# Kernel tuning notes

Measured on AMD Instinct MI355X. Metric: run time of the kernel, lower is better.

Reference implementation:

```python
import jax, jax.numpy as jnp
import numpy as np

HIDDEN = 1024
NUM_HEADS = 16
HEAD_DIM = HIDDEN // NUM_HEADS


def setup_inputs() -> dict:
    key = jax.random.key(0)
    ks = jax.random.split(key, 13)
    B, S, H = 4, 2048, HIDDEN
    sc = 1.0 / np.sqrt(H)
    inp = {
        'queries': jax.random.normal(ks[0], (B, S, H), jnp.float32),
        'keys': jax.random.normal(ks[1], (B, S, H), jnp.float32),
        'values': jax.random.normal(ks[2], (B, S, H), jnp.float32),
        'attention_mask': jax.random.randint(ks[3], (B, S, S), 0, 2, jnp.int32),
        'W_q': jax.random.normal(ks[4], (H, H), jnp.float32) * sc,
        'b_q': jnp.zeros((H,), jnp.float32),
        'W_k': jax.random.normal(ks[5], (H, H), jnp.float32) * sc,
        'b_k': jnp.zeros((H,), jnp.float32),
        'W_v': jax.random.normal(ks[6], (H, H), jnp.float32) * sc,
        'b_v': jnp.zeros((H,), jnp.float32),
        'W_o': jax.random.normal(ks[7], (H, H), jnp.float32) * sc,
        'b_o': jnp.zeros((H,), jnp.float32),
    }
    return inp


def _split_heads(x):
    # [B, S, H] -> [B, nH, S, d]
    B, S, _ = x.shape
    return x.reshape(B, S, NUM_HEADS, HEAD_DIM).transpose(0, 2, 1, 3)


def reference(queries, keys, values, attention_mask, W_q, b_q, W_k, b_k, W_v, b_v, W_o, b_o):
    q = _split_heads(queries @ W_q + b_q)   # [B, nH, S, d]
    k = _split_heads(keys @ W_k + b_k)
    v = _split_heads(values @ W_v + b_v)
    d = q.shape[-1]
    scores = jnp.einsum('bhqd,bhkd->bhqk', q, k) / jnp.sqrt(jnp.float32(d))
    # mask repeat_interleave over heads == broadcast mask over head axis
    mask = attention_mask[:, None, :, :]    # [B, 1, S, S]
    scores = jnp.where(mask == 0, jnp.float32(-1e6), scores)
    attn = jax.nn.softmax(scores, axis=-1)  # dropout p=0 -> identity
    out = jnp.einsum('bhqk,bhkd->bhqd', attn, v)  # [B, nH, S, d]
    B, _, S, _ = out.shape
    out = out.transpose(0, 2, 1, 3).reshape(B, S, NUM_HEADS * HEAD_DIM)
    return out @ W_o + b_o
```

## Files before the change

kernel.cpp:

```cpp
#include <hip/hip_runtime.h>
#include <stdint.h>

typedef unsigned short u16;
typedef uint32_t u32;
typedef unsigned long long u64;
typedef short bf16x8 __attribute__((ext_vector_type(8)));
typedef float f32x4 __attribute__((ext_vector_type(4)));
typedef float f32x16 __attribute__((ext_vector_type(16)));

#define MFMA16 __builtin_amdgcn_mfma_f32_16x16x32_bf16
#define MFMA32 __builtin_amdgcn_mfma_f32_32x32x16_bf16
#define L2E 1.44269504088896340736f

static __device__ __forceinline__ u16 f2bf(float f) {
  union { float f; u32 u; } v; v.f = f;
  u32 r = v.u + 0x7FFFu + ((v.u >> 16) & 1u);
  return (u16)(r >> 16);
}

static __device__ __forceinline__ u32 cvtpk(float lo, float hi) {
  u32 r;
  asm("v_cvt_pk_bf16_f32 %0, %1, %2" : "=v"(r) : "v"(lo), "v"(hi));
  return r;
}

static __device__ __forceinline__ void glds16(const u16* g, u16* l) {
  __builtin_amdgcn_global_load_lds((const __attribute__((address_space(1))) void*)g,
                                   (__attribute__((address_space(3))) void*)l, 16, 0, 0);
}

__global__ __launch_bounds__(256) void cvt3_kernel(
    const float* __restrict__ s0, const float* __restrict__ s1, const float* __restrict__ s2,
    u16* __restrict__ d0, u16* __restrict__ d1, u16* __restrict__ d2) {
  const float* s = (blockIdx.z == 0) ? s0 : (blockIdx.z == 1) ? s1 : s2;
  u16* d = (blockIdx.z == 0) ? d0 : (blockIdx.z == 1) ? d1 : d2;
  size_t i = ((size_t)blockIdx.x * 256 + threadIdx.x) * 8;
  float4 a = *(const float4*)(s + i);
  float4 c = *(const float4*)(s + i + 4);
  bf16x8 o;
  o[0] = (short)f2bf(a.x); o[1] = (short)f2bf(a.y);
  o[2] = (short)f2bf(a.z); o[3] = (short)f2bf(a.w);
  o[4] = (short)f2bf(c.x); o[5] = (short)f2bf(c.y);
  o[6] = (short)f2bf(c.z); o[7] = (short)f2bf(c.w);
  *(bf16x8*)(d + i) = o;
}

__global__ __launch_bounds__(256) void wtrans_kernel(
    const float* __restrict__ w0, const float* __restrict__ w1,
    const float* __restrict__ w2, const float* __restrict__ w3,
    u16* __restrict__ t0, u16* __restrict__ t1, u16* __restrict__ t2, u16* __restrict__ t3) {
  const float* w = (blockIdx.z == 0) ? w0 : (blockIdx.z == 1) ? w1 : (blockIdx.z == 2) ? w2 : w3;
  u16* t = (blockIdx.z == 0) ? t0 : (blockIdx.z == 1) ? t1 : (blockIdx.z == 2) ? t2 : t3;
  __shared__ float tile[64][65];
  const int bx = blockIdx.x, by = blockIdx.y;
#pragma unroll
  for (int i = 0; i < 16; ++i) {
    int idx = i * 256 + threadIdx.x;
    int r = idx >> 6, c = idx & 63;
    tile[r][c] = w[(size_t)(by * 64 + r) * 1024 + bx * 64 + c];
  }
  __syncthreads();
#pragma unroll
  for (int i = 0; i < 16; ++i) {
    int idx = i * 256 + threadIdx.x;
    int r = idx >> 6, c = idx & 63;
    t[(size_t)(bx * 64 + r) * 1024 + by * 64 + c] = f2bf(tile[c][r]);
  }
}

__global__ __launch_bounds__(256) void packmask_kernel(const int* __restrict__ m,
                                                       u32* __restrict__ pmo) {
  const size_t i = (size_t)blockIdx.x * 256 + threadIdx.x;
  const int lane = threadIdx.x & 63;
  unsigned long long b = __ballot(m[i] != 0);
  if (lane == 0) pmo[i >> 5] = (u32)b;
  else if (lane == 32) pmo[i >> 5] = (u32)(b >> 32);
}

template <int OM>
__global__ __launch_bounds__(512, 2) void gemm_kernel(
    const u16* __restrict__ A, const u16* __restrict__ Bt, const float* __restrict__ bias,
    void* __restrict__ Cout, float oscale) {
  constexpr int K = 1024, N = 1024;
  constexpr int NT = K / 64;
  __shared__ u16 As[3][256 * 64];
  __shared__ u16 Bs[3][128 * 64];
  const int tid = threadIdx.x;
  const int lane = tid & 63;
  const int wid = tid >> 6;
  const int l15 = lane & 15;
  const int lg = lane >> 4;
  const int row0 = blockIdx.x * 256;
  const int col0 = blockIdx.y * 128;
  const int wr = wid >> 1, wc = wid & 1;
  const int swf = (l15 & 7) << 3;
  const f32x4 fzero = {0.f, 0.f, 0.f, 0.f};

  f32x4 acc[4][4];
#pragma unroll
  for (int m = 0; m < 4; ++m)
#pragma unroll
    for (int n = 0; n < 4; ++n) acc[m][n] = fzero;

#define GSTAGE(buf, k0)                                                        \
  do {                                                                         \
    _Pragma("unroll") for (int i = 0; i < 4; ++i) {                            \
      int e = (i * 512 + tid) * 8;                                             \
      int r = e >> 6, c = e & 63;                                              \
      int cs = c ^ ((r & 7) << 3);                                             \
      glds16(A + (size_t)(row0 + r) * K + (k0) + cs, &As[buf][e]);             \
    }                                                                          \
    _Pragma("unroll") for (int i = 0; i < 2; ++i) {                            \
      int e = (i * 512 + tid) * 8;                                             \
      int r = e >> 6, c = e & 63;                                              \
      int cs = c ^ ((r & 7) << 3);                                             \
      glds16(Bt + (size_t)(col0 + r) * K + (k0) + cs, &Bs[buf][e]);            \
    }                                                                          \
  } while (0)

  GSTAGE(0, 0);
  GSTAGE(1, 64);
  asm volatile("s_waitcnt vmcnt(6)" ::: "memory");
  __builtin_amdgcn_s_barrier();
  __builtin_amdgcn_sched_barrier(0);

  for (int t = 0; t < NT; ++t) {
    const int buf = t % 3;
    if (t + 2 < NT) GSTAGE((t + 2) % 3, (t + 2) * 64);

    __builtin_amdgcn_s_setprio(1);
#pragma unroll
    for (int ks = 0; ks < 2; ++ks) {
      const int koff = ks * 32 + lg * 8;
      bf16x8 af[4], bfr[4];
#pragma unroll
      for (int m = 0; m < 4; ++m)
        af[m] = *(const bf16x8*)(&As[buf][(wr * 64 + m * 16 + l15) * 64 + (koff ^ swf)]);
#pragma unroll
      for (int n = 0; n < 4; ++n)
        bfr[n] = *(const bf16x8*)(&Bs[buf][(wc * 64 + n * 16 + l15) * 64 + (koff ^ swf)]);
#pragma unroll
      for (int m = 0; m < 4; ++m)
#pragma unroll
        for (int n = 0; n < 4; ++n)
          acc[m][n] = MFMA16(af[m], bfr[n], acc[m][n], 0, 0, 0);
    }
    __builtin_amdgcn_s_setprio(0);

    if (t + 1 < NT) {
      if (t + 2 < NT)
        asm volatile("s_waitcnt vmcnt(6)" ::: "memory");
      else
        asm volatile("s_waitcnt vmcnt(0)" ::: "memory");
      __builtin_amdgcn_s_barrier();
      __builtin_amdgcn_sched_barrier(0);
    }
  }
#undef GSTAGE

#pragma unroll
  for (int n = 0; n < 4; ++n) {
    const int col = col0 + wc * 64 + n * 16 + l15;
    const float bv = bias[col];
#pragma unroll
    for (int m = 0; m < 4; ++m) {
#pragma unroll
      for (int r = 0; r < 4; ++r) {
        const int row = row0 + wr * 64 + m * 16 + lg * 4 + r;
        const float v = (acc[m][n][r] + bv) * oscale;
        if constexpr (OM == 0) {
          ((u16*)Cout)[(size_t)row * N + col] = f2bf(v);
        } else if constexpr (OM == 1) {
          ((float*)Cout)[(size_t)row * N + col] = v;
        } else {
          const int b_ = row >> 11, s_ = row & 2047, h_ = col >> 6, d_ = col & 63;
          ((u16*)Cout)[(size_t)((b_ * 16 + h_) * 64 + d_) * 2048 + s_] = f2bf(v);
        }
      }
    }
  }
}

__global__ __launch_bounds__(256, 4) void attn_kernel(
    const u16* __restrict__ Qb, const u16* __restrict__ Kb, const u16* __restrict__ Vt,
    const u32* __restrict__ pm, u16* __restrict__ Oa) {
  __shared__ u16 Ks[2][64 * 64];
  __shared__ u16 Vs[2][64 * 64];
  __shared__ uint4 mlut[16];
  const int tid = threadIdx.x;
  const int lane = tid & 63;
  const int wid = tid >> 6;
  const int c31 = lane & 31;
  const int hi = lane >> 5;
  const int qt = blockIdx.x;
  const int hh = blockIdx.y;
  const int bb = blockIdx.z;
  const int qbase = qt * 128 + wid * 32;
  const int sw = (lane & 7) << 3;

  if (tid < 16)
    mlut[tid] = make_uint4((u32) - (int)(tid & 1), (u32) - (int)((tid >> 1) & 1),
                           (u32) - (int)((tid >> 2) & 1), (u32) - (int)((tid >> 3) & 1));

  const size_t qrow = (size_t)(bb * 2048 + qbase + c31);
  bf16x8 qf[4];
#pragma unroll
  for (int ds = 0; ds < 4; ++ds)
    qf[ds] = *(const bf16x8*)(Qb + qrow * 1024 + hh * 64 + ds * 16 + hi * 8);

  float lrun = 0.f;
  f32x16 oacc[2];
#pragma unroll
  for (int dn = 0; dn < 2; ++dn)
#pragma unroll
    for (int r = 0; r < 16; ++r) oacc[dn][r] = 0.f;

  const size_t kgbase = (size_t)(bb * 2048) * 1024 + hh * 64;
  const size_t vgbase = (size_t)((bb * 16 + hh) * 64) * 2048;

#define STAGE(buf, kbase)                                                              \
  do {                                                                                 \
    _Pragma("unroll") for (int i = 0; i < 2; ++i) {                                    \
      int r = ((i * 256 + tid) * 8) >> 6, c = ((i * 256 + tid) * 8) & 63;              \
      int cs = c ^ ((r & 7) << 3);                                                     \
      glds16(Kb + kgbase + (size_t)((kbase) + r) * 1024 + cs,                          \
             &Ks[buf][(i * 256 + wid * 64) * 8]);                                      \
      glds16(Vt + vgbase + (size_t)r * 2048 + (kbase) + cs,                            \
             &Vs[buf][(i * 256 + wid * 64) * 8]);                                      \
    }                                                                                  \
  } while (0)

  STAGE(0, 0);
  __syncthreads();

  int cur = 0;
  for (int kt = 0; kt < 32; ++kt) {
    if (kt < 31) STAGE(cur ^ 1, (kt + 1) * 64);

    const u64 mw = *(const u64*)(pm + qrow * 64 + kt * 2);
    float ps = 0.f;

#pragma unroll
    for (int kb = 0; kb < 2; ++kb) {
      f32x16 sacc;
#pragma unroll
      for (int r = 0; r < 16; ++r) sacc[r] = 0.f;
#pragma unroll
      for (int ds = 0; ds < 4; ++ds) {
        bf16x8 kf = *(const bf16x8*)(&Ks[cur][(kb * 32 + c31) * 64 + ((ds * 16 + hi * 8) ^ sw)]);
        sacc = MFMA32(kf, qf[ds], sacc, 0, 0, 0);
      }

      const u32 mwk = (u32)(mw >> (kb * 32));
      u32 Ap[4], Bp[4];
#pragma unroll
      for (int q2 = 0; q2 < 4; ++q2) {
        const u32 kb4 = (mwk >> (q2 * 8 + hi * 4)) & 0xFu;
        const uint4 mm = mlut[kb4];
        const float p0 = __builtin_amdgcn_exp2f(sacc[4 * q2 + 0]);
        const float p1 = __builtin_amdgcn_exp2f(sacc[4 * q2 + 1]);
        const float p2 = __builtin_amdgcn_exp2f(sacc[4 * q2 + 2]);
        const float p3 = __builtin_amdgcn_exp2f(sacc[4 * q2 + 3]);
        const float f0 = __uint_as_float(__float_as_uint(p0) & mm.x);
        const float f1 = __uint_as_float(__float_as_uint(p1) & mm.y);
        const float f2 = __uint_as_float(__float_as_uint(p2) & mm.z);
        const float f3 = __uint_as_float(__float_as_uint(p3) & mm.w);
        ps += (f0 + f1) + (f2 + f3);
        Ap[q2] = cvtpk(f0, f1);
        Bp[q2] = cvtpk(f2, f3);
      }

      asm("v_permlane32_swap_b32 %0, %1" : "+v"(Ap[0]), "+v"(Ap[1]));
      asm("v_permlane32_swap_b32 %0, %1" : "+v"(Bp[0]), "+v"(Bp[1]));
      asm("v_permlane32_swap_b32 %0, %1" : "+v"(Ap[2]), "+v"(Ap[3]));
      asm("v_permlane32_swap_b32 %0, %1" : "+v"(Bp[2]), "+v"(Bp[3]));

#pragma unroll
      for (int t = 0; t < 2; ++t) {
        uint4 fr;
        fr.x = Ap[2 * t]; fr.y = Bp[2 * t]; fr.z = Ap[2 * t + 1]; fr.w = Bp[2 * t + 1];
        const bf16x8 pf = *(const bf16x8*)&fr;
        const int koff = (kb * 2 + t) * 16 + hi * 8;
#pragma unroll
        for (int dn = 0; dn < 2; ++dn) {
          bf16x8 vf = *(const bf16x8*)(&Vs[cur][(dn * 32 + c31) * 64 + (koff ^ sw)]);
          oacc[dn] = MFMA32(vf, pf, oacc[dn], 0, 0, 0);
        }
      }
    }

    ps += __shfl_xor(ps, 32);
    lrun += ps;

    __syncthreads();
    cur ^= 1;
  }
#undef STAGE

  const float inv = 1.0f / lrun;
  u16* orow = Oa + qrow * 1024 + hh * 64;
#pragma unroll
  for (int dn = 0; dn < 2; ++dn) {
#pragma unroll
    for (int q2 = 0; q2 < 4; ++q2) {
      uint2 w;
      w.x = cvtpk(oacc[dn][4 * q2 + 0] * inv, oacc[dn][4 * q2 + 1] * inv);
      w.y = cvtpk(oacc[dn][4 * q2 + 2] * inv, oacc[dn][4 * q2 + 3] * inv);
      *(uint2*)(orow + dn * 32 + q2 * 8 + hi * 4) = w;
    }
  }
}

extern "C" void kernel_launch(void* const* d_in, const int* in_sizes, int n_in,
                              void* d_out, int out_size, void* d_ws, size_t ws_size,
                              hipStream_t stream) {
  const float* q = (const float*)d_in[0];
  const float* k = (const float*)d_in[1];
  const float* v = (const float*)d_in[2];
  const int* mask = (const int*)d_in[3];
  const float* Wq = (const float*)d_in[4]; const float* bq = (const float*)d_in[5];
  const float* Wk = (const float*)d_in[6]; const float* bk = (const float*)d_in[7];
  const float* Wv = (const float*)d_in[8]; const float* bv = (const float*)d_in[9];
  const float* Wo = (const float*)d_in[10]; const float* bo = (const float*)d_in[11];
  float* out = (float*)d_out;
  char* ws = (char*)d_ws;
  const size_t MB = 1024ull * 1024ull;
  u16* qbf = (u16*)(ws + 0 * MB);
  u16* kbf = (u16*)(ws + 16 * MB);
  u16* vbf = (u16*)(ws + 32 * MB);
  u16* Qp  = (u16*)(ws + 48 * MB);
  u16* Kp  = (u16*)(ws + 64 * MB);
  u16* Vtp = (u16*)(ws + 80 * MB);
  u16* Wqt = (u16*)(ws + 96 * MB);
  u16* Wkt = (u16*)(ws + 98 * MB);
  u16* Wvt = (u16*)(ws + 100 * MB);
  u16* Wot = (u16*)(ws + 102 * MB);
  u32* pmb = (u32*)(ws + 104 * MB);
  u16* Oa  = qbf;

  const float QSCALE = 0.125f * L2E;

  cvt3_kernel<<<dim3(4096, 1, 3), 256, 0, stream>>>(q, k, v, qbf, kbf, vbf);
  wtrans_kernel<<<dim3(16, 16, 4), 256, 0, stream>>>(Wq, Wk, Wv, Wo, Wqt, Wkt, Wvt, Wot);
  packmask_kernel<<<dim3(65536), 256, 0, stream>>>(mask, pmb);
  gemm_kernel<0><<<dim3(32, 8), 512, 0, stream>>>(qbf, Wqt, bq, Qp, QSCALE);
  gemm_kernel<0><<<dim3(32, 8), 512, 0, stream>>>(kbf, Wkt, bk, Kp, 1.0f);
  gemm_kernel<2><<<dim3(32, 8), 512, 0, stream>>>(vbf, Wvt, bv, Vtp, 1.0f);
  attn_kernel<<<dim3(16, 16, 4), 256, 0, stream>>>(Qp, Kp, Vtp, pmb, Oa);
  gemm_kernel<1><<<dim3(32, 8), 512, 0, stream>>>(Oa, Wot, bo, out, 1.0f);
}
```

Baseline: 267.6 us.

## Fuse fp32-to-bf16 input conversion into projection GEMM A-tile loads

```diff
diff --git a/kernel.cpp b/kernel.cpp
--- a/kernel.cpp
+++ b/kernel.cpp
@@ -27,22 +27,6 @@
 static __device__ __forceinline__ void glds16(const u16* g, u16* l) {
   __builtin_amdgcn_global_load_lds((const __attribute__((address_space(1))) void*)g,
                                    (__attribute__((address_space(3))) void*)l, 16, 0, 0);
-}
-
-__global__ __launch_bounds__(256) void cvt3_kernel(
-    const float* __restrict__ s0, const float* __restrict__ s1, const float* __restrict__ s2,
-    u16* __restrict__ d0, u16* __restrict__ d1, u16* __restrict__ d2) {
-  const float* s = (blockIdx.z == 0) ? s0 : (blockIdx.z == 1) ? s1 : s2;
-  u16* d = (blockIdx.z == 0) ? d0 : (blockIdx.z == 1) ? d1 : d2;
-  size_t i = ((size_t)blockIdx.x * 256 + threadIdx.x) * 8;
-  float4 a = *(const float4*)(s + i);
-  float4 c = *(const float4*)(s + i + 4);
-  bf16x8 o;
-  o[0] = (short)f2bf(a.x); o[1] = (short)f2bf(a.y);
-  o[2] = (short)f2bf(a.z); o[3] = (short)f2bf(a.w);
-  o[4] = (short)f2bf(c.x); o[5] = (short)f2bf(c.y);
-  o[6] = (short)f2bf(c.z); o[7] = (short)f2bf(c.w);
-  *(bf16x8*)(d + i) = o;
 }
 
 __global__ __launch_bounds__(256) void wtrans_kernel(
@@ -79,12 +63,15 @@
 
 template <int OM>
 __global__ __launch_bounds__(512, 2) void gemm_kernel(
-    const u16* __restrict__ A, const u16* __restrict__ Bt, const float* __restrict__ bias,
+    const void* __restrict__ Apv, const u16* __restrict__ Bt, const float* __restrict__ bias,
     void* __restrict__ Cout, float oscale) {
   constexpr int K = 1024, N = 1024;
   constexpr int NT = K / 64;
+  constexpr bool AF32 = (OM != 1);
   __shared__ u16 As[3][256 * 64];
   __shared__ u16 Bs[3][128 * 64];
+  const u16* Ab = (const u16*)Apv;
+  const float* Af = (const float*)Apv;
   const int tid = threadIdx.x;
   const int lane = tid & 63;
   const int wid = tid >> 6;
@@ -102,14 +89,10 @@
 #pragma unroll
     for (int n = 0; n < 4; ++n) acc[m][n] = fzero;
 
-#define GSTAGE(buf, k0)                                                        \
+  float4 aA[8], aB[8];
+
+#define BGLDS(buf, k0)                                                         \
   do {                                                                         \
-    _Pragma("unroll") for (int i = 0; i < 4; ++i) {                            \
-      int e = (i * 512 + tid) * 8;                                             \
-      int r = e >> 6, c = e & 63;                                              \
-      int cs = c ^ ((r & 7) << 3);                                             \
-      glds16(A + (size_t)(row0 + r) * K + (k0) + cs, &As[buf][e]);             \
-    }                                                                          \
     _Pragma("unroll") for (int i = 0; i < 2; ++i) {                            \
       int e = (i * 512 + tid) * 8;                                             \
       int r = e >> 6, c = e & 63;                                              \
@@ -118,45 +101,130 @@
     }                                                                          \
   } while (0)
 
-  GSTAGE(0, 0);
-  GSTAGE(1, 64);
-  asm volatile("s_waitcnt vmcnt(6)" ::: "memory");
-  __builtin_amdgcn_s_barrier();
-  __builtin_amdgcn_sched_barrier(0);
-
-  for (int t = 0; t < NT; ++t) {
-    const int buf = t % 3;
-    if (t + 2 < NT) GSTAGE((t + 2) % 3, (t + 2) * 64);
-
-    __builtin_amdgcn_s_setprio(1);
-#pragma unroll
-    for (int ks = 0; ks < 2; ++ks) {
-      const int koff = ks * 32 + lg * 8;
-      bf16x8 af[4], bfr[4];
-#pragma unroll
-      for (int m = 0; m < 4; ++m)
-        af[m] = *(const bf16x8*)(&As[buf][(wr * 64 + m * 16 + l15) * 64 + (koff ^ swf)]);
-#pragma unroll
-      for (int n = 0; n < 4; ++n)
-        bfr[n] = *(const bf16x8*)(&Bs[buf][(wc * 64 + n * 16 + l15) * 64 + (koff ^ swf)]);
-#pragma unroll
-      for (int m = 0; m < 4; ++m)
-#pragma unroll
-        for (int n = 0; n < 4; ++n)
-          acc[m][n] = MFMA16(af[m], bfr[n], acc[m][n], 0, 0, 0);
+#define GSTAGE_BF(buf, k0)                                                     \
+  do {                                                                         \
+    _Pragma("unroll") for (int i = 0; i < 4; ++i) {                            \
+      int e = (i * 512 + tid) * 8;                                             \
+      int r = e >> 6, c = e & 63;                                              \
+      int cs = c ^ ((r & 7) << 3);                                             \
+      glds16(Ab + (size_t)(row0 + r) * K + (k0) + cs, &As[buf][e]);            \
+    }                                                                          \
+    BGLDS(buf, k0);                                                            \
+  } while (0)
+
+#define GISSUE(areg, bufB, k0)                                                 \
+  do {                                                                         \
+    _Pragma("unroll") for (int i = 0; i < 4; ++i) {                            \
+      int e = (i * 512 + tid) * 8;                                             \
+      int r = e >> 6, c = e & 63;                                              \
+      const float* src = Af + (size_t)(row0 + r) * K + (k0) + c;               \
+      areg[2 * i] = *(const float4*)src;                                       \
+      areg[2 * i + 1] = *(const float4*)(src + 4);                             \
+    }                                                                          \
+    BGLDS(bufB, k0);                                                           \
+  } while (0)
+
+#define AWRITE(areg, bufw)                                                     \
+  do {                                                                         \
+    _Pragma("unroll") for (int i = 0; i < 4; ++i) {                            \
+      int e = (i * 512 + tid) * 8;                                             \
+      int r = e >> 6, c = e & 63;                                              \
+      int cs = c ^ ((r & 7) << 3);                                             \
+      uint4 w;                                                                 \
+      w.x = cvtpk(areg[2 * i].x, areg[2 * i].y);                               \
+      w.y = cvtpk(areg[2 * i].z, areg[2 * i].w);                               \
+      w.z = cvtpk(areg[2 * i + 1].x, areg[2 * i + 1].y);                       \
+      w.w = cvtpk(areg[2 * i + 1].z, areg[2 * i + 1].w);                       \
+      *(uint4*)(&As[bufw][r * 64 + cs]) = w;                                   \
+    }                                                                          \
+  } while (0)
+
+#define COMPUTE(buf)                                                           \
+  do {                                                                         \
+    __builtin_amdgcn_s_setprio(1);                                             \
+    _Pragma("unroll") for (int ks = 0; ks < 2; ++ks) {                         \
+      const int koff = ks * 32 + lg * 8;                                       \
+      bf16x8 af[4], bfr[4];                                                    \
+      _Pragma("unroll") for (int m = 0; m < 4; ++m)                            \
+        af[m] = *(const bf16x8*)(&As[buf][(wr * 64 + m * 16 + l15) * 64 +      \
+                                          (koff ^ swf)]);                      \
+      _Pragma("unroll") for (int n = 0; n < 4; ++n)                            \
+        bfr[n] = *(const bf16x8*)(&Bs[buf][(wc * 64 + n * 16 + l15) * 64 +     \
+                                           (koff ^ swf)]);                     \
+      _Pragma("unroll") for (int m = 0; m < 4; ++m)                            \
+        _Pragma("unroll") for (int n = 0; n < 4; ++n)                          \
+          acc[m][n] = MFMA16(af[m], bfr[n], acc[m][n], 0, 0, 0);               \
+    }                                                                          \
+    __builtin_amdgcn_s_setprio(0);                                             \
+  } while (0)
+
+  if constexpr (AF32) {
+    GISSUE(aA, 0, 0);
+    GISSUE(aB, 1, 64);
+    asm volatile("s_waitcnt vmcnt(10)" ::: "memory");
+    AWRITE(aA, 0);
+    asm volatile("s_waitcnt lgkmcnt(0)" ::: "memory");
+    __builtin_amdgcn_s_barrier();
+    __builtin_amdgcn_sched_barrier(0);
+
+    for (int t = 0; t < NT; t += 2) {
+      {
+        if (t + 2 < NT) GISSUE(aA, (t + 2) % 3, (t + 2) * 64);
+        __builtin_amdgcn_sched_barrier(0);
+        COMPUTE(t % 3);
+        if (t + 2 < NT)
+          asm volatile("s_waitcnt vmcnt(10)" ::: "memory");
+        else
+          asm volatile("s_waitcnt vmcnt(0)" ::: "memory");
+        AWRITE(aB, (t + 1) % 3);
+        asm volatile("s_waitcnt lgkmcnt(0)" ::: "memory");
+        __builtin_amdgcn_s_barrier();
+        __builtin_amdgcn_sched_barrier(0);
+      }
+      {
+        const int t1 = t + 1;
+        if (t1 + 2 < NT) GISSUE(aB, (t1 + 2) % 3, (t1 + 2) * 64);
+        __builtin_amdgcn_sched_barrier(0);
+        COMPUTE(t1 % 3);
+        if (t1 + 1 < NT) {
+          if (t1 + 2 < NT)
+            asm volatile("s_waitcnt vmcnt(10)" ::: "memory");
+          else
+            asm volatile("s_waitcnt vmcnt(0)" ::: "memory");
+          AWRITE(aA, (t1 + 1) % 3);
+          asm volatile("s_waitcnt lgkmcnt(0)" ::: "memory");
+          __builtin_amdgcn_s_barrier();
+          __builtin_amdgcn_sched_barrier(0);
+        }
+      }
     }
-    __builtin_amdgcn_s_setprio(0);
-
-    if (t + 1 < NT) {
-      if (t + 2 < NT)
-        asm volatile("s_waitcnt vmcnt(6)" ::: "memory");
-      else
-        asm volatile("s_waitcnt vmcnt(0)" ::: "memory");
-      __builtin_amdgcn_s_barrier();
+  } else {
+    GSTAGE_BF(0, 0);
+    GSTAGE_BF(1, 64);
+    asm volatile("s_waitcnt vmcnt(6)" ::: "memory");
+    __builtin_amdgcn_s_barrier();
+    __builtin_amdgcn_sched_barrier(0);
+
+    for (int t = 0; t < NT; ++t) {
+      const int buf = t % 3;
+      if (t + 2 < NT) GSTAGE_BF((t + 2) % 3, (t + 2) * 64);
       __builtin_amdgcn_sched_barrier(0);
+      COMPUTE(buf);
+      if (t + 1 < NT) {
+        if (t + 2 < NT)
+          asm volatile("s_waitcnt vmcnt(6)" ::: "memory");
+        else
+          asm volatile("s_waitcnt vmcnt(0)" ::: "memory");
+        __builtin_amdgcn_s_barrier();
+        __builtin_amdgcn_sched_barrier(0);
+      }
     }
   }
-#undef GSTAGE
+#undef BGLDS
+#undef GSTAGE_BF
+#undef GISSUE
+#undef AWRITE
+#undef COMPUTE
 
 #pragma unroll
   for (int n = 0; n < 4; ++n) {
@@ -325,9 +393,7 @@
   float* out = (float*)d_out;
   char* ws = (char*)d_ws;
   const size_t MB = 1024ull * 1024ull;
-  u16* qbf = (u16*)(ws + 0 * MB);
-  u16* kbf = (u16*)(ws + 16 * MB);
-  u16* vbf = (u16*)(ws + 32 * MB);
+  u16* Oa  = (u16*)(ws + 0 * MB);
   u16* Qp  = (u16*)(ws + 48 * MB);
   u16* Kp  = (u16*)(ws + 64 * MB);
   u16* Vtp = (u16*)(ws + 80 * MB);
@@ -336,16 +402,14 @@
   u16* Wvt = (u16*)(ws + 100 * MB);
   u16* Wot = (u16*)(ws + 102 * MB);
   u32* pmb = (u32*)(ws + 104 * MB);
-  u16* Oa  = qbf;
 
   const float QSCALE = 0.125f * L2E;
 
-  cvt3_kernel<<<dim3(4096, 1, 3), 256, 0, stream>>>(q, k, v, qbf, kbf, vbf);
   wtrans_kernel<<<dim3(16, 16, 4), 256, 0, stream>>>(Wq, Wk, Wv, Wo, Wqt, Wkt, Wvt, Wot);
   packmask_kernel<<<dim3(65536), 256, 0, stream>>>(mask, pmb);
-  gemm_kernel<0><<<dim3(32, 8), 512, 0, stream>>>(qbf, Wqt, bq, Qp, QSCALE);
-  gemm_kernel<0><<<dim3(32, 8), 512, 0, stream>>>(kbf, Wkt, bk, Kp, 1.0f);
-  gemm_kernel<2><<<dim3(32, 8), 512, 0, stream>>>(vbf, Wvt, bv, Vtp, 1.0f);
+  gemm_kernel<0><<<dim3(32, 8), 512, 0, stream>>>(q, Wqt, bq, Qp, QSCALE);
+  gemm_kernel<0><<<dim3(32, 8), 512, 0, stream>>>(k, Wkt, bk, Kp, 1.0f);
+  gemm_kernel<2><<<dim3(32, 8), 512, 0, stream>>>(v, Wvt, bv, Vtp, 1.0f);
   attn_kernel<<<dim3(16, 16, 4), 256, 0, stream>>>(Qp, Kp, Vtp, pmb, Oa);
   gemm_kernel<1><<<dim3(32, 8), 512, 0, stream>>>(Oa, Wot, bo, out, 1.0f);
 }
```

Result: no change. 271.0 us (+1.3%).
